# Optimization experiments

Measured on AMD Instinct MI355X. Metric: run time of the kernel, lower is better.

## Reference

```python
import jax, jax.numpy as jnp
import numpy as np

SR = 44100  # sample_rate from __init__


def setup_inputs() -> dict:
    key = jax.random.key(0)
    k1, k2 = jax.random.split(key)
    x = jax.random.normal(k1, (64, 2, 131072), dtype=jnp.float32) * 0.1
    t = jax.random.uniform(k2, (64,), dtype=jnp.float32)
    filter_freq = jnp.array([1000.0], dtype=jnp.float32)  # learnable param
    filter_q = jnp.array([0.707], dtype=jnp.float32)      # learnable param
    return {"x": x, "t": t, "filter_freq": filter_freq, "filter_q": filter_q}


def _highpass_biquad(x, filter_freq, filter_q):
    # parameter clamping as in the module's forward
    freq = jnp.clip(filter_freq, 100.0, SR / 2.0 - 1.0)[0]
    q = jnp.clip(filter_q, 0.1, 10.0)[0]
    # torchaudio highpass_biquad coefficients
    w0 = 2.0 * jnp.pi * freq / SR
    cosw = jnp.cos(w0)
    alpha = jnp.sin(w0) / (2.0 * q)
    a0 = 1.0 + alpha
    b0 = ((1.0 + cosw) * 0.5) / a0
    b1 = (-(1.0 + cosw)) / a0
    b2 = b0
    a1 = (-2.0 * cosw) / a0
    a2 = (1.0 - alpha) / a0
    # FIR (feedforward) part, zero initial conditions: fused elementwise
    x1 = jnp.pad(x, ((0, 0), (0, 0), (1, 0)))[..., :-1]
    x2 = jnp.pad(x, ((0, 0), (0, 0), (2, 0)))[..., :-2]
    xf = b0 * x + b1 * x1 + b2 * x2  # [B, C, T]
    # IIR (feedback) 2nd-order recurrence over time, vectorized over (B, C)
    xf_t = jnp.moveaxis(xf, -1, 0)  # [T, B, C]

    def step(carry, u):
        y1, y2 = carry
        y = u - a1 * y1 - a2 * y2
        return (y, y1), y

    zero = jnp.zeros(xf_t.shape[1:], xf_t.dtype)
    _, ys = jax.lax.scan(step, (zero, zero), xf_t)
    y = jnp.moveaxis(ys, 0, -1)  # [B, C, T]
    # torchaudio lfilter default clamp=True
    return jnp.clip(y, -1.0, 1.0)


def reference(x, t, filter_freq, filter_q):
    # t is accepted but unused, matching the original forward signature
    return _highpass_biquad(x, filter_freq, filter_q)
```

## Files before the change

### kernel.cpp

```cpp
#include <hip/hip_runtime.h>
#include <math.h>


constexpr int T_LEN  = 131072;
constexpr int L      = 64;
constexpr int CPB    = 64;
constexpr int SEG    = CPB * L;
constexpr int SPB    = 4;
constexpr int GRP_PER_SEQ = T_LEN / (SEG * SPB);
constexpr int NSEQ   = 64 * 2;
constexpr int NBLOCKS = NSEQ * GRP_PER_SEQ;

typedef float fx4 __attribute__((ext_vector_type(4)));

#define AS1(p) ((const __attribute__((address_space(1))) void*)(p))
#define AS3(p) ((__attribute__((address_space(3))) void*)(p))

__global__ __launch_bounds__(64) void hp_kernel(
    const float* __restrict__ x,
    const float* __restrict__ pfreq,
    const float* __restrict__ pq,
    float* __restrict__ out)
{
    __shared__ fx4 lds4[2][CPB * 16];

    float freq = fminf(fmaxf(pfreq[0], 100.0f), 44100.0f * 0.5f - 1.0f);
    float q    = fminf(fmaxf(pq[0], 0.1f), 10.0f);
    float w0   = 2.0f * (float)M_PI * freq / 44100.0f;
    float cw   = cosf(w0);
    float alpha = sinf(w0) / (2.0f * q);
    float ia0  = 1.0f / (1.0f + alpha);
    const float b0 = (1.0f + cw) * 0.5f * ia0;
    const float b1 = -(1.0f + cw) * ia0;
    const float b2 = b0;
    const float a1 = -2.0f * cw * ia0;
    const float a2 = (1.0f - alpha) * ia0;

    const int borig = blockIdx.x;
    const int b     = ((borig & 7) << 7) | (borig >> 3);

    const int seq = b >> 3;
    const int S0  = (b & (GRP_PER_SEQ - 1)) * (SEG * SPB);
    const float* __restrict__ xs = x   + (size_t)seq * T_LEN;
    float*       __restrict__ os = out + (size_t)seq * T_LEN;
    const int tid = threadIdx.x;

    float hp1 = 0.f, hp2 = 0.f;
    if (S0 > 0 && tid < 2) {
        const float* w = xs + S0 + (tid - 1) * L;
        hp1 = w[-1]; hp2 = w[-2];
    }
    fx4 h[16];
    if (S0 > 0 && tid == 0) {
        const fx4* gw = (const fx4*)(xs + S0 - L);
#pragma unroll
        for (int k = 0; k < 16; ++k) h[k] = gw[k];
    }

#pragma unroll
    for (int k = 0; k < 16; ++k) {
        int s4 = tid + (k << 6);
        int r  = s4 >> 4;
        int g  = (r << 4) | ((s4 & 15) ^ (r & 15));
        __builtin_amdgcn_global_load_lds(AS1(xs + S0 + (g << 2)),
                                         AS3(&lds4[0][k << 6]), 16, 0, 0);
    }
#pragma unroll
    for (int k = 0; k < 16; ++k) {
        int s4 = tid + (k << 6);
        int r  = s4 >> 4;
        int g  = (r << 4) | ((s4 & 15) ^ (r & 15));
        __builtin_amdgcn_global_load_lds(AS1(xs + S0 + SEG + (g << 2)),
                                         AS3(&lds4[1][k << 6]), 16, 0, 0);
    }

    float ny1 = 0.f, ny2 = 0.f, np1 = 0.f, np2 = 0.f;

#define STEP(xv) { \
        float xf_ = fmaf(b2, p2, fmaf(b1, p1, b0 * (xv))); \
        float yv  = fmaf(-a1, y1, fmaf(-a2, y2, xf_)); \
        p2 = p1; p1 = (xv); y2 = y1; y1 = yv; }

#pragma unroll 1
    for (int s = 0; s < SPB; ++s) {
        const int S = S0 + s * SEG;
        fx4* buf = lds4[s & 1];

        asm volatile("s_waitcnt vmcnt(16) lgkmcnt(0)" ::: "memory");
        __builtin_amdgcn_sched_barrier(0);

        if (s >= 1 && s + 1 < SPB) {
            fx4* nb = lds4[(s + 1) & 1];
            const float* gseg = xs + S + SEG;
#pragma unroll
            for (int k = 0; k < 16; ++k) {
                int s4 = tid + (k << 6);
                int r  = s4 >> 4;
                int g  = (r << 4) | ((s4 & 15) ^ (r & 15));
                __builtin_amdgcn_global_load_lds(AS1(gseg + (g << 2)),
                                                 AS3(&nb[k << 6]), 16, 0, 0);
            }
        }

        float y1, y2, p1, p2;

        if (s == 0) {
            y1 = 0.f; y2 = 0.f; p1 = 0.f; p2 = 0.f;
            const int cgm = (S0 >> 6) + tid;
            if (cgm >= 1) {
                if (cgm >= 2) {
                    if (tid >= 2) {
                        int rr = tid - 2;
                        const float* pr = (const float*)
                            (buf + ((rr << 4) | (15 ^ (rr & 15))));
                        p2 = pr[2]; p1 = pr[3];
                    } else { p1 = hp1; p2 = hp2; }
                }
                const fx4* rp = buf + (((tid - 1) & 63) << 4);
                const int  xr = (tid - 1) & 15;
#pragma unroll
                for (int j4 = 0; j4 < 16; ++j4) {
                    fx4 v = (tid == 0) ? h[j4] : rp[j4 ^ xr];
                    STEP(v.x); STEP(v.y); STEP(v.z); STEP(v.w);
                }
            }
        } else {
            if (tid == 0) {
                y1 = ny1; y2 = ny2; p1 = np1; p2 = np2;
            } else {
                y1 = 0.f; y2 = 0.f;
                if (tid >= 2) {
                    int rr = tid - 2;
                    const float* pr = (const float*)
                        (buf + ((rr << 4) | (15 ^ (rr & 15))));
                    p2 = pr[2]; p1 = pr[3];
                } else { p1 = np1; p2 = np2; }
                const fx4* rp = buf + ((tid - 1) << 4);
                const int  xr = (tid - 1) & 15;
#pragma unroll
                for (int j4 = 0; j4 < 16; ++j4) {
                    fx4 v = rp[j4 ^ xr];
                    STEP(v.x); STEP(v.y); STEP(v.z); STEP(v.w);
                }
            }
        }

        {
            fx4* mrow = buf + (tid << 4);
            const int xm = tid & 15;
#pragma unroll
            for (int j4 = 0; j4 < 16; ++j4) {
                int idx = j4 ^ xm;
                fx4 v = mrow[idx];
                fx4 o;
                STEP(v.x); o.x = fminf(fmaxf(y1, -1.f), 1.f);
                STEP(v.y); o.y = fminf(fmaxf(y1, -1.f), 1.f);
                STEP(v.z); o.z = fminf(fmaxf(y1, -1.f), 1.f);
                STEP(v.w); o.w = fminf(fmaxf(y1, -1.f), 1.f);
                mrow[idx] = o;
            }
        }

        ny1 = __shfl(y1, 63); ny2 = __shfl(y2, 63);
        np1 = __shfl(p1, 63); np2 = __shfl(p2, 63);

        {
            fx4* ob = (fx4*)(os + S);
#pragma unroll
            for (int k = 0; k < 16; ++k) {
                int f = tid + (k << 6);
                int r = f >> 4;
                fx4 v = buf[(r << 4) | ((f & 15) ^ (r & 15))];
                __builtin_nontemporal_store(v, &ob[f]);
            }
        }
    }
#undef STEP
}

extern "C" void kernel_launch(void* const* d_in, const int* in_sizes, int n_in,
                              void* d_out, int out_size, void* d_ws, size_t ws_size,
                              hipStream_t stream) {
    const float* x  = (const float*)d_in[0];
    const float* ff = (const float*)d_in[2];
    const float* fq = (const float*)d_in[3];
    float* out = (float*)d_out;
    hp_kernel<<<NBLOCKS, CPB, 0, stream>>>(x, ff, fq, out);
}
```

Baseline: 115.7 us.

## Load both segments into registers upfront and halve segments per block

```diff
diff --git a/kernel.cpp b/kernel.cpp
--- a/kernel.cpp
+++ b/kernel.cpp
@@ -6,15 +6,12 @@
 constexpr int L      = 64;
 constexpr int CPB    = 64;
 constexpr int SEG    = CPB * L;
-constexpr int SPB    = 4;
+constexpr int SPB    = 2;
 constexpr int GRP_PER_SEQ = T_LEN / (SEG * SPB);
 constexpr int NSEQ   = 64 * 2;
 constexpr int NBLOCKS = NSEQ * GRP_PER_SEQ;
 
 typedef float fx4 __attribute__((ext_vector_type(4)));
-
-#define AS1(p) ((const __attribute__((address_space(1))) void*)(p))
-#define AS3(p) ((__attribute__((address_space(3))) void*)(p))
 
 __global__ __launch_bounds__(64) void hp_kernel(
     const float* __restrict__ x,
@@ -22,7 +19,7 @@
     const float* __restrict__ pq,
     float* __restrict__ out)
 {
-    __shared__ fx4 lds4[2][CPB * 16];
+    __shared__ fx4 lds4[CPB * 16];
 
     float freq = fminf(fmaxf(pfreq[0], 100.0f), 44100.0f * 0.5f - 1.0f);
     float q    = fminf(fmaxf(pq[0], 0.1f), 10.0f);
@@ -37,13 +34,20 @@
     const float a2 = (1.0f - alpha) * ia0;
 
     const int borig = blockIdx.x;
-    const int b     = ((borig & 7) << 7) | (borig >> 3);
+    const int b     = ((borig & 7) << 8) | (borig >> 3);
 
-    const int seq = b >> 3;
+    const int seq = b >> 4;
     const int S0  = (b & (GRP_PER_SEQ - 1)) * (SEG * SPB);
     const float* __restrict__ xs = x   + (size_t)seq * T_LEN;
     float*       __restrict__ os = out + (size_t)seq * T_LEN;
     const int tid = threadIdx.x;
+
+    const fx4* g0 = (const fx4*)(xs + S0);
+    fx4 a[16], bb[16];
+#pragma unroll
+    for (int k = 0; k < 16; ++k) a[k]  = g0[tid + (k << 6)];
+#pragma unroll
+    for (int k = 0; k < 16; ++k) bb[k] = g0[1024 + tid + (k << 6)];
 
     float hp1 = 0.f, hp2 = 0.f;
     if (S0 > 0 && tid < 2) {
@@ -56,97 +60,46 @@
 #pragma unroll
         for (int k = 0; k < 16; ++k) h[k] = gw[k];
     }
-
-#pragma unroll
-    for (int k = 0; k < 16; ++k) {
-        int s4 = tid + (k << 6);
-        int r  = s4 >> 4;
-        int g  = (r << 4) | ((s4 & 15) ^ (r & 15));
-        __builtin_amdgcn_global_load_lds(AS1(xs + S0 + (g << 2)),
-                                         AS3(&lds4[0][k << 6]), 16, 0, 0);
-    }
-#pragma unroll
-    for (int k = 0; k < 16; ++k) {
-        int s4 = tid + (k << 6);
-        int r  = s4 >> 4;
-        int g  = (r << 4) | ((s4 & 15) ^ (r & 15));
-        __builtin_amdgcn_global_load_lds(AS1(xs + S0 + SEG + (g << 2)),
-                                         AS3(&lds4[1][k << 6]), 16, 0, 0);
-    }
-
-    float ny1 = 0.f, ny2 = 0.f, np1 = 0.f, np2 = 0.f;
+    __builtin_amdgcn_sched_barrier(0);
 
 #define STEP(xv) { \
         float xf_ = fmaf(b2, p2, fmaf(b1, p1, b0 * (xv))); \
         float yv  = fmaf(-a1, y1, fmaf(-a2, y2, xf_)); \
         p2 = p1; p1 = (xv); y2 = y1; y1 = yv; }
 
-#pragma unroll 1
-    for (int s = 0; s < SPB; ++s) {
-        const int S = S0 + s * SEG;
-        fx4* buf = lds4[s & 1];
+    float ny1, ny2, np1, np2;
 
-        asm volatile("s_waitcnt vmcnt(16) lgkmcnt(0)" ::: "memory");
-        __builtin_amdgcn_sched_barrier(0);
-
-        if (s >= 1 && s + 1 < SPB) {
-            fx4* nb = lds4[(s + 1) & 1];
-            const float* gseg = xs + S + SEG;
+    {
 #pragma unroll
-            for (int k = 0; k < 16; ++k) {
-                int s4 = tid + (k << 6);
-                int r  = s4 >> 4;
-                int g  = (r << 4) | ((s4 & 15) ^ (r & 15));
-                __builtin_amdgcn_global_load_lds(AS1(gseg + (g << 2)),
-                                                 AS3(&nb[k << 6]), 16, 0, 0);
-            }
+        for (int k = 0; k < 16; ++k) {
+            int g = tid + (k << 6);
+            int r = g >> 4;
+            lds4[(r << 4) | ((g & 15) ^ (r & 15))] = a[k];
         }
 
-        float y1, y2, p1, p2;
+        float y1 = 0.f, y2 = 0.f, p1 = 0.f, p2 = 0.f;
 
-        if (s == 0) {
-            y1 = 0.f; y2 = 0.f; p1 = 0.f; p2 = 0.f;
-            const int cgm = (S0 >> 6) + tid;
-            if (cgm >= 1) {
-                if (cgm >= 2) {
-                    if (tid >= 2) {
-                        int rr = tid - 2;
-                        const float* pr = (const float*)
-                            (buf + ((rr << 4) | (15 ^ (rr & 15))));
-                        p2 = pr[2]; p1 = pr[3];
-                    } else { p1 = hp1; p2 = hp2; }
-                }
-                const fx4* rp = buf + (((tid - 1) & 63) << 4);
-                const int  xr = (tid - 1) & 15;
-#pragma unroll
-                for (int j4 = 0; j4 < 16; ++j4) {
-                    fx4 v = (tid == 0) ? h[j4] : rp[j4 ^ xr];
-                    STEP(v.x); STEP(v.y); STEP(v.z); STEP(v.w);
-                }
-            }
-        } else {
-            if (tid == 0) {
-                y1 = ny1; y2 = ny2; p1 = np1; p2 = np2;
-            } else {
-                y1 = 0.f; y2 = 0.f;
+        const int cgm = (S0 >> 6) + tid;
+        if (cgm >= 1) {
+            if (cgm >= 2) {
                 if (tid >= 2) {
                     int rr = tid - 2;
                     const float* pr = (const float*)
-                        (buf + ((rr << 4) | (15 ^ (rr & 15))));
+                        (lds4 + ((rr << 4) | (15 ^ (rr & 15))));
                     p2 = pr[2]; p1 = pr[3];
-                } else { p1 = np1; p2 = np2; }
-                const fx4* rp = buf + ((tid - 1) << 4);
-                const int  xr = (tid - 1) & 15;
+                } else { p1 = hp1; p2 = hp2; }
+            }
+            const fx4* rp = lds4 + (((tid - 1) & 63) << 4);
+            const int  xr = (tid - 1) & 15;
 #pragma unroll
-                for (int j4 = 0; j4 < 16; ++j4) {
-                    fx4 v = rp[j4 ^ xr];
-                    STEP(v.x); STEP(v.y); STEP(v.z); STEP(v.w);
-                }
+            for (int j4 = 0; j4 < 16; ++j4) {
+                fx4 v = (tid == 0) ? h[j4] : rp[j4 ^ xr];
+                STEP(v.x); STEP(v.y); STEP(v.z); STEP(v.w);
             }
         }
 
         {
-            fx4* mrow = buf + (tid << 4);
+            fx4* mrow = lds4 + (tid << 4);
             const int xm = tid & 15;
 #pragma unroll
             for (int j4 = 0; j4 < 16; ++j4) {
@@ -165,12 +118,68 @@
         np1 = __shfl(p1, 63); np2 = __shfl(p2, 63);
 
         {
-            fx4* ob = (fx4*)(os + S);
+            fx4* ob = (fx4*)(os + S0);
 #pragma unroll
             for (int k = 0; k < 16; ++k) {
                 int f = tid + (k << 6);
                 int r = f >> 4;
-                fx4 v = buf[(r << 4) | ((f & 15) ^ (r & 15))];
+                fx4 v = lds4[(r << 4) | ((f & 15) ^ (r & 15))];
+                __builtin_nontemporal_store(v, &ob[f]);
+            }
+        }
+    }
+
+    {
+#pragma unroll
+        for (int k = 0; k < 16; ++k) {
+            int g = tid + (k << 6);
+            int r = g >> 4;
+            lds4[(r << 4) | ((g & 15) ^ (r & 15))] = bb[k];
+        }
+
+        float y1, y2, p1, p2;
+        if (tid == 0) {
+            y1 = ny1; y2 = ny2; p1 = np1; p2 = np2;
+        } else {
+            y1 = 0.f; y2 = 0.f;
+            if (tid >= 2) {
+                int rr = tid - 2;
+                const float* pr = (const float*)
+                    (lds4 + ((rr << 4) | (15 ^ (rr & 15))));
+                p2 = pr[2]; p1 = pr[3];
+            } else { p1 = np1; p2 = np2; }
+            const fx4* rp = lds4 + ((tid - 1) << 4);
+            const int  xr = (tid - 1) & 15;
+#pragma unroll
+            for (int j4 = 0; j4 < 16; ++j4) {
+                fx4 v = rp[j4 ^ xr];
+                STEP(v.x); STEP(v.y); STEP(v.z); STEP(v.w);
+            }
+        }
+
+        {
+            fx4* mrow = lds4 + (tid << 4);
+            const int xm = tid & 15;
+#pragma unroll
+            for (int j4 = 0; j4 < 16; ++j4) {
+                int idx = j4 ^ xm;
+                fx4 v = mrow[idx];
+                fx4 o;
+                STEP(v.x); o.x = fminf(fmaxf(y1, -1.f), 1.f);
+                STEP(v.y); o.y = fminf(fmaxf(y1, -1.f), 1.f);
+                STEP(v.z); o.z = fminf(fmaxf(y1, -1.f), 1.f);
+                STEP(v.w); o.w = fminf(fmaxf(y1, -1.f), 1.f);
+                mrow[idx] = o;
+            }
+        }
+
+        {
+            fx4* ob = (fx4*)(os + S0 + SEG);
+#pragma unroll
+            for (int k = 0; k < 16; ++k) {
+                int f = tid + (k << 6);
+                int r = f >> 4;
+                fx4 v = lds4[(r << 4) | ((f & 15) ^ (r & 15))];
                 __builtin_nontemporal_store(v, &ob[f]);
             }
         }
```

New measurement: 117.5 us. Within noise of the previous version (+1.6%).

## Halve per-thread chunk length and use two-chunk warm-up to double block count

Applied to the files above, without the earlier changes.

```diff
diff --git a/kernel.cpp b/kernel.cpp
--- a/kernel.cpp
+++ b/kernel.cpp
@@ -3,18 +3,21 @@
 
 
 constexpr int T_LEN  = 131072;
-constexpr int L      = 64;
+constexpr int L      = 32;
 constexpr int CPB    = 64;
 constexpr int SEG    = CPB * L;
 constexpr int SPB    = 4;
-constexpr int GRP_PER_SEQ = T_LEN / (SEG * SPB);
+constexpr int GRP    = SEG * SPB;
+constexpr int GRP_PER_SEQ = T_LEN / GRP;
 constexpr int NSEQ   = 64 * 2;
 constexpr int NBLOCKS = NSEQ * GRP_PER_SEQ;
+constexpr int RPF    = L / 4;
 
 typedef float fx4 __attribute__((ext_vector_type(4)));
 
 #define AS1(p) ((const __attribute__((address_space(1))) void*)(p))
 #define AS3(p) ((__attribute__((address_space(3))) void*)(p))
+#define SLOT(r, p) ((((r) & 63) << 3) | ((p) ^ ((r) & 7)))
 
 __global__ __launch_bounds__(64) void hp_kernel(
     const float* __restrict__ x,
@@ -22,7 +25,7 @@
     const float* __restrict__ pq,
     float* __restrict__ out)
 {
-    __shared__ fx4 lds4[2][CPB * 16];
+    __shared__ fx4 lds4[2][CPB * RPF];
 
     float freq = fminf(fmaxf(pfreq[0], 100.0f), 44100.0f * 0.5f - 1.0f);
     float q    = fminf(fmaxf(pq[0], 0.1f), 10.0f);
@@ -37,120 +40,135 @@
     const float a2 = (1.0f - alpha) * ia0;
 
     const int borig = blockIdx.x;
-    const int b     = ((borig & 7) << 7) | (borig >> 3);
-
-    const int seq = b >> 3;
-    const int S0  = (b & (GRP_PER_SEQ - 1)) * (SEG * SPB);
+    const int b     = ((borig & 7) << 8) | (borig >> 3);
+
+    const int seq = b >> 4;
+    const int S0  = (b & (GRP_PER_SEQ - 1)) * GRP;
     const float* __restrict__ xs = x   + (size_t)seq * T_LEN;
     float*       __restrict__ os = out + (size_t)seq * T_LEN;
     const int tid = threadIdx.x;
 
     float hp1 = 0.f, hp2 = 0.f;
+    if (S0 > 0 && tid < 3) {
+        const float* wb = xs + S0 - 64 + (tid << 5);
+        hp1 = wb[-1]; hp2 = wb[-2];
+    }
+    fx4 hh[16];
+#pragma unroll
+    for (int k = 0; k < 16; ++k) hh[k] = fx4{0.f, 0.f, 0.f, 0.f};
     if (S0 > 0 && tid < 2) {
-        const float* w = xs + S0 + (tid - 1) * L;
-        hp1 = w[-1]; hp2 = w[-2];
-    }
-    fx4 h[16];
-    if (S0 > 0 && tid == 0) {
-        const fx4* gw = (const fx4*)(xs + S0 - L);
-#pragma unroll
-        for (int k = 0; k < 16; ++k) h[k] = gw[k];
-    }
-
-#pragma unroll
-    for (int k = 0; k < 16; ++k) {
-        int s4 = tid + (k << 6);
-        int r  = s4 >> 4;
-        int g  = (r << 4) | ((s4 & 15) ^ (r & 15));
+        const fx4* gw = (const fx4*)(xs + S0 - 64 + (tid << 5));
+#pragma unroll
+        for (int k = 0; k < 16; ++k) hh[k] = gw[k];
+    }
+
+#pragma unroll
+    for (int k = 0; k < 8; ++k) {
+        int s4 = (k << 6) + tid;
+        int r  = s4 >> 3;
+        int g  = (r << 3) | ((s4 & 7) ^ (r & 7));
         __builtin_amdgcn_global_load_lds(AS1(xs + S0 + (g << 2)),
                                          AS3(&lds4[0][k << 6]), 16, 0, 0);
     }
 #pragma unroll
-    for (int k = 0; k < 16; ++k) {
-        int s4 = tid + (k << 6);
-        int r  = s4 >> 4;
-        int g  = (r << 4) | ((s4 & 15) ^ (r & 15));
+    for (int k = 0; k < 8; ++k) {
+        int s4 = (k << 6) + tid;
+        int r  = s4 >> 3;
+        int g  = (r << 3) | ((s4 & 7) ^ (r & 7));
         __builtin_amdgcn_global_load_lds(AS1(xs + S0 + SEG + (g << 2)),
                                          AS3(&lds4[1][k << 6]), 16, 0, 0);
     }
 
     float ny1 = 0.f, ny2 = 0.f, np1 = 0.f, np2 = 0.f;
+    float mp1 = 0.f, mp2 = 0.f;
 
 #define STEP(xv) { \
         float xf_ = fmaf(b2, p2, fmaf(b1, p1, b0 * (xv))); \
         float yv  = fmaf(-a1, y1, fmaf(-a2, y2, xf_)); \
         p2 = p1; p1 = (xv); y2 = y1; y1 = yv; }
+#define STEP4(v) { STEP((v).x); STEP((v).y); STEP((v).z); STEP((v).w); }
 
 #pragma unroll 1
     for (int s = 0; s < SPB; ++s) {
         const int S = S0 + s * SEG;
         fx4* buf = lds4[s & 1];
-
-        asm volatile("s_waitcnt vmcnt(16) lgkmcnt(0)" ::: "memory");
+        fx4* nb  = lds4[(s & 1) ^ 1];
+
+        asm volatile("s_waitcnt vmcnt(8) lgkmcnt(0)" ::: "memory");
         __builtin_amdgcn_sched_barrier(0);
 
         if (s >= 1 && s + 1 < SPB) {
-            fx4* nb = lds4[(s + 1) & 1];
             const float* gseg = xs + S + SEG;
 #pragma unroll
-            for (int k = 0; k < 16; ++k) {
-                int s4 = tid + (k << 6);
-                int r  = s4 >> 4;
-                int g  = (r << 4) | ((s4 & 15) ^ (r & 15));
+            for (int k = 0; k < 8; ++k) {
+                int s4 = (k << 6) + tid;
+                int r  = s4 >> 3;
+                int g  = (r << 3) | ((s4 & 7) ^ (r & 7));
                 __builtin_amdgcn_global_load_lds(AS1(gseg + (g << 2)),
                                                  AS3(&nb[k << 6]), 16, 0, 0);
             }
         }
 
         float y1, y2, p1, p2;
+        const int rm2 = (tid - 2) & 63, rm1 = (tid - 1) & 63;
 
         if (s == 0) {
             y1 = 0.f; y2 = 0.f; p1 = 0.f; p2 = 0.f;
-            const int cgm = (S0 >> 6) + tid;
-            if (cgm >= 1) {
-                if (cgm >= 2) {
-                    if (tid >= 2) {
-                        int rr = tid - 2;
-                        const float* pr = (const float*)
-                            (buf + ((rr << 4) | (15 ^ (rr & 15))));
-                        p2 = pr[2]; p1 = pr[3];
-                    } else { p1 = hp1; p2 = hp2; }
+            const int cg = (S0 >> 5) + tid;
+            if (cg >= 1) {
+                if (tid >= 3) {
+                    const float* pr = (const float*)(buf + SLOT(tid - 3, 7));
+                    p2 = pr[2]; p1 = pr[3];
+                } else { p1 = hp1; p2 = hp2; }
+#pragma unroll
+                for (int j = 0; j < 8; ++j) {
+                    fx4 lv = buf[SLOT(rm2, j)];
+                    fx4 v = (tid < 2) ? hh[j] : lv;
+                    STEP4(v);
                 }
-                const fx4* rp = buf + (((tid - 1) & 63) << 4);
-                const int  xr = (tid - 1) & 15;
-#pragma unroll
-                for (int j4 = 0; j4 < 16; ++j4) {
-                    fx4 v = (tid == 0) ? h[j4] : rp[j4 ^ xr];
-                    STEP(v.x); STEP(v.y); STEP(v.z); STEP(v.w);
+#pragma unroll
+                for (int j = 0; j < 8; ++j) {
+                    fx4 lv = buf[SLOT(rm1, j)];
+                    fx4 v = (tid < 2 && S0 > 0) ? hh[j + 8] : lv;
+                    STEP4(v);
                 }
             }
         } else {
+            y1 = 0.f; y2 = 0.f;
+            if (tid >= 3) {
+                const float* pr = (const float*)(buf + SLOT(tid - 3, 7));
+                p2 = pr[2]; p1 = pr[3];
+            } else {
+                p1 = (tid == 1) ? mp1 : np1;
+                p2 = (tid == 1) ? mp2 : np2;
+            }
+#pragma unroll
+            for (int j = 0; j < 8; ++j) {
+                fx4 lv = buf[SLOT(rm2, j)];
+                fx4 v = (tid < 2) ? hh[j] : lv;
+                STEP4(v);
+            }
+#pragma unroll
+            for (int j = 0; j < 8; ++j) {
+                fx4 v = buf[SLOT(rm1, j)];
+                STEP4(v);
+            }
             if (tid == 0) {
                 y1 = ny1; y2 = ny2; p1 = np1; p2 = np2;
-            } else {
-                y1 = 0.f; y2 = 0.f;
-                if (tid >= 2) {
-                    int rr = tid - 2;
-                    const float* pr = (const float*)
-                        (buf + ((rr << 4) | (15 ^ (rr & 15))));
-                    p2 = pr[2]; p1 = pr[3];
-                } else { p1 = np1; p2 = np2; }
-                const fx4* rp = buf + ((tid - 1) << 4);
-                const int  xr = (tid - 1) & 15;
-#pragma unroll
-                for (int j4 = 0; j4 < 16; ++j4) {
-                    fx4 v = rp[j4 ^ xr];
-                    STEP(v.x); STEP(v.y); STEP(v.z); STEP(v.w);
-                }
-            }
+            }
+        }
+
+        if (s + 1 < SPB && tid < 2) {
+#pragma unroll
+            for (int j = 0; j < 8; ++j) hh[j] = buf[SLOT(63, j)];
         }
 
         {
-            fx4* mrow = buf + (tid << 4);
-            const int xm = tid & 15;
-#pragma unroll
-            for (int j4 = 0; j4 < 16; ++j4) {
-                int idx = j4 ^ xm;
+            fx4* mrow = buf + (tid << 3);
+            const int xm = tid & 7;
+#pragma unroll
+            for (int j = 0; j < 8; ++j) {
+                int idx = j ^ xm;
                 fx4 v = mrow[idx];
                 fx4 o;
                 STEP(v.x); o.x = fminf(fmaxf(y1, -1.f), 1.f);
@@ -163,18 +181,20 @@
 
         ny1 = __shfl(y1, 63); ny2 = __shfl(y2, 63);
         np1 = __shfl(p1, 63); np2 = __shfl(p2, 63);
+        mp1 = __shfl(p1, 62); mp2 = __shfl(p2, 62);
 
         {
             fx4* ob = (fx4*)(os + S);
 #pragma unroll
-            for (int k = 0; k < 16; ++k) {
-                int f = tid + (k << 6);
-                int r = f >> 4;
-                fx4 v = buf[(r << 4) | ((f & 15) ^ (r & 15))];
+            for (int k = 0; k < 8; ++k) {
+                int f = (k << 6) + tid;
+                int r = f >> 3;
+                fx4 v = buf[(r << 3) | ((f & 7) ^ (r & 7))];
                 __builtin_nontemporal_store(v, &ob[f]);
             }
         }
     }
+#undef STEP4
 #undef STEP
 }
 
```

After: 114.1 us. Within noise of the previous version (-1.3%).
